# Kernel optimization log

Measured on AMD Instinct MI355X. Metric: run time of the kernel, lower is better.

The kernel has to match this reference:

```python
import jax, jax.numpy as jnp
import numpy as np

B, T, C, H = 2, 2048, 768, 12
HD = C // H  # head dim = 64


def setup_inputs() -> dict:
    key = jax.random.key(0)
    k1, k2, k3 = jax.random.split(key, 3)
    s_in = 1.0 / np.sqrt(C)
    return {
        "x": jax.random.normal(k1, (B, T, C), dtype=jnp.float32),
        "Wqkv": jax.random.normal(k2, (C, 3 * C), dtype=jnp.float32) * s_in,
        "bqkv": jnp.zeros((3 * C,), dtype=jnp.float32),
        "Wproj": jax.random.normal(k3, (C, C), dtype=jnp.float32) * s_in,
        "bproj": jnp.zeros((C,), dtype=jnp.float32),
    }


def reference(x, Wqkv, bqkv, Wproj, bproj):
    b, t, c = x.shape
    qkv = x @ Wqkv + bqkv                      # [b, t, 3c]
    q, k, v = jnp.split(qkv, 3, axis=2)
    # [b, h, t, hd]
    q = q.reshape(b, t, H, HD).transpose(0, 2, 1, 3)
    k = k.reshape(b, t, H, HD).transpose(0, 2, 1, 3)
    v = v.reshape(b, t, H, HD).transpose(0, 2, 1, 3)
    scale = 1.0 / np.sqrt(HD)
    att = jnp.einsum("bhqd,bhkd->bhqk", q, k) * scale  # [b, h, t, t]
    causal = jnp.tril(jnp.ones((t, t), dtype=bool))
    att = jnp.where(causal[None, None], att, -jnp.inf)
    att = jax.nn.softmax(att, axis=-1)
    y = jnp.einsum("bhqk,bhkd->bhqd", att, v)          # [b, h, t, hd]
    y = y.transpose(0, 2, 1, 3).reshape(b, t, c)
    return y @ Wproj + bproj
```

## Files before the change

kernel.cpp:

```cpp
#include <hip/hip_runtime.h>
#include <math.h>

#define BB 2
#define TT 2048
#define CC 768
#define HH 12
#define HD 64
#define N3 (3*CC)

typedef __attribute__((ext_vector_type(8))) short short8;
typedef __attribute__((ext_vector_type(8))) _Float16 f16x8;
typedef __attribute__((ext_vector_type(4))) float f32x4;
typedef unsigned short u16;

#define QSCALE 0.1803368809f

static __device__ __forceinline__ u16 f2h(float x) {
    union { _Float16 h; u16 u; } v; v.h = (_Float16)x; return v.u;
}
static __device__ __forceinline__ float ex2(float x) {
#if __has_builtin(__builtin_amdgcn_exp2f)
    return __builtin_amdgcn_exp2f(x);
#else
    return exp2f(x);
#endif
}
static __device__ __forceinline__ unsigned pk2h(float a, float b) {
    auto p = __builtin_amdgcn_cvt_pkrtz(a, b);
    return __builtin_bit_cast(unsigned, p);
}

static __device__ __forceinline__ void gl16(const void* g, void* l) {
    __builtin_amdgcn_global_load_lds(
        (const __attribute__((address_space(1))) void*)g,
        (__attribute__((address_space(3))) void*)l, 16, 0, 0);
}

__global__ __launch_bounds__(256)
void conv_all(const float* __restrict__ x, u16* __restrict__ xh,
              const float* __restrict__ Wq, u16* __restrict__ wqh,
              const float* __restrict__ Wp, u16* __restrict__ wph)
{
    __shared__ float Tt[64][65];
    const int b = blockIdx.x;
    if (b < 3072) {
        const int i = b * 256 + threadIdx.x;
        float4 v = ((const float4*)x)[i];
        ushort4 o;
        o.x = f2h(v.x); o.y = f2h(v.y); o.z = f2h(v.z); o.w = f2h(v.w);
        ((ushort4*)xh)[i] = o;
        return;
    }
    const float* W; u16* T; int N, idx;
    if (b < 3504) { W = Wq; T = wqh; N = N3; idx = b - 3072; }
    else          { W = Wp; T = wph; N = CC; idx = b - 3504; }
    const int ntx = N / 64;
    const int n0 = (idx % ntx) * 64, k0 = (idx / ntx) * 64;
    const int tid = threadIdx.x;
    {
        const int r = tid >> 2, q = tid & 3;
        #pragma unroll
        for (int i = 0; i < 4; ++i) {
            float4 v = *(const float4*)(W + (size_t)(k0 + r) * N + n0 + q * 16 + i * 4);
            Tt[q * 16 + i * 4 + 0][r] = v.x;
            Tt[q * 16 + i * 4 + 1][r] = v.y;
            Tt[q * 16 + i * 4 + 2][r] = v.z;
            Tt[q * 16 + i * 4 + 3][r] = v.w;
        }
    }
    __syncthreads();
    {
        const int n = tid >> 2, q = tid & 3;
        u16 hh[16];
        #pragma unroll
        for (int j = 0; j < 16; ++j) hh[j] = f2h(Tt[n][q * 16 + j]);
        u16* dh = T + (size_t)(n0 + n) * 768 + k0 + q * 16;
        *(short8*)(dh) = *(short8*)&hh[0];
        *(short8*)(dh + 8) = *(short8*)&hh[8];
    }
}

template<int NCOLS, int MODE>
__global__ __launch_bounds__(256)
void mm3(const u16* __restrict__ A_g, const u16* __restrict__ B_g,
         const float* __restrict__ bias, float* __restrict__ outF,
         u16* __restrict__ qo, u16* __restrict__ ko, u16* __restrict__ vto)
{
    __shared__ u16 gsm[16384];
    char* smb = (char*)gsm;
    const int tid = threadIdx.x, lane = tid & 63, wv = tid >> 6;
    const int wm = wv >> 1, wn = wv & 1, r16 = lane & 15, kg = lane >> 4;
    const int m0 = blockIdx.y * 128, n0 = blockIdx.x * 128;

    const u16 *pA[2], *pB[2];
    int ldsq[2];
    #pragma unroll
    for (int qq = 0; qq < 2; ++qq) {
        const int L = wv * 2048 + qq * 1024 + lane * 16;
        const int row = L >> 6, c = (L >> 4) & 3;
        const int cp = c ^ ((row >> 1) & 3);
        ldsq[qq] = wv * 2048 + qq * 1024;
        pA[qq] = A_g + (size_t)(m0 + row) * 768 + cp * 8;
        pB[qq] = B_g + (size_t)(n0 + row) * 768 + cp * 8;
    }

    int aA[4], aB[4];
    #pragma unroll
    for (int t = 0; t < 4; ++t) {
        const int rA = wm * 64 + t * 16 + r16;
        const int rB = wn * 64 + t * 16 + r16;
        aA[t] = rA * 64 + ((kg ^ ((rA >> 1) & 3)) << 4);
        aB[t] = rB * 64 + ((kg ^ ((rB >> 1) & 3)) << 4) + 8192;
    }

    f32x4 acc[4][4];
    #pragma unroll
    for (int i = 0; i < 4; ++i)
        #pragma unroll
        for (int j = 0; j < 4; ++j) acc[i][j] = (f32x4)0.f;

    #pragma unroll
    for (int qq = 0; qq < 2; ++qq) {
        gl16(pA[qq], smb + ldsq[qq]);
        gl16(pB[qq], smb + 8192 + ldsq[qq]);
        pA[qq] += 32; pB[qq] += 32;
    }
    __syncthreads();

    int cur = 0;
    for (int ks = 0; ks < 24; ++ks) {
        const int nxt = cur ^ 1;
        if (ks != 23) {
            #pragma unroll
            for (int qq = 0; qq < 2; ++qq) {
                gl16(pA[qq], smb + nxt * 16384 + ldsq[qq]);
                gl16(pB[qq], smb + nxt * 16384 + 8192 + ldsq[qq]);
                pA[qq] += 32; pB[qq] += 32;
            }
        }
        const int cb = cur * 16384;
        f16x8 a[4], b[4];
        #pragma unroll
        for (int t = 0; t < 4; ++t) {
            a[t] = *(const f16x8*)(smb + cb + aA[t]);
            b[t] = *(const f16x8*)(smb + cb + aB[t]);
        }
        #pragma unroll
        for (int mt = 0; mt < 4; ++mt)
            #pragma unroll
            for (int nt = 0; nt < 4; ++nt)
                acc[mt][nt] = __builtin_amdgcn_mfma_f32_16x16x32_f16(a[mt], b[nt], acc[mt][nt], 0, 0, 0);
        __syncthreads();
        cur = nxt;
    }

    float bi[4];
    #pragma unroll
    for (int nt = 0; nt < 4; ++nt) bi[nt] = bias[n0 + wn * 64 + nt * 16 + r16];

    if (MODE == 1) {
        #pragma unroll
        for (int mt = 0; mt < 4; ++mt)
            #pragma unroll
            for (int nt = 0; nt < 4; ++nt)
                #pragma unroll
                for (int r = 0; r < 4; ++r) {
                    const int grow = m0 + wm * 64 + mt * 16 + kg * 4 + r;
                    const int gcol = n0 + wn * 64 + nt * 16 + r16;
                    outF[(size_t)grow * CC + gcol] = acc[mt][nt][r] + bi[nt];
                }
    } else {
        const int which = n0 / CC;
        const float qsc = (which == 0) ? QSCALE : 1.0f;
        const int b_ = m0 >> 11;
        #pragma unroll
        for (int mt = 0; mt < 4; ++mt) {
            const int tb = ((m0 & 2047) + wm * 64 + mt * 16 + kg * 4);
            #pragma unroll
            for (int nt = 0; nt < 4; ++nt) {
                const int gcol = n0 + wn * 64 + nt * 16 + r16;
                const int cc = gcol - which * CC;
                const int h = cc >> 6, d = cc & 63;
                const int bh_ = b_ * HH + h;
                if (which == 2) {
                    ushort4 hv;
                    #pragma unroll
                    for (int r = 0; r < 4; ++r)
                        ((u16*)&hv)[r] = f2h(acc[mt][nt][r] + bi[nt]);
                    *(ushort4*)(vto + ((size_t)bh_ * 64 + d) * 2048 + tb) = hv;
                } else {
                    u16* dst = (which == 0) ? qo : ko;
                    #pragma unroll
                    for (int r = 0; r < 4; ++r)
                        dst[(((size_t)bh_ * 2048 + tb + r) << 6) + d] =
                            f2h((acc[mt][nt][r] + bi[nt]) * qsc);
                }
            }
        }
    }
}

__global__ __launch_bounds__(256)
void attn3(const u16* __restrict__ qp, const u16* __restrict__ kp,
           const u16* __restrict__ vtp, u16* __restrict__ attp)
{
    __shared__ u16 smem[24576];
    char* smb = (char*)smem;

    const int tid = threadIdx.x, bid = blockIdx.x;
    const int qt = 15 - (bid / 24);
    const int bh = bid % 24;
    const int t0 = qt * 128;
    const int jmax = 2 * qt + 1;
    const int diagA = 2 * qt;
    const int lane = tid & 63, wv = tid >> 6;
    const int r16 = lane & 15, kg = lane >> 4;
    const int r7 = r16 & 7;
    const int kg8 = kg * 8, kg4 = kg * 4;

    const size_t qroA = ((size_t)bh * TT + t0 + wv * 16 + r16) * 64;
    f16x8 qfA[2], qfB[2];
    #pragma unroll
    for (int ks = 0; ks < 2; ++ks) {
        qfA[ks] = *(const f16x8*)(qp + qroA + ks * 32 + kg8);
        qfB[ks] = *(const f16x8*)(qp + qroA + 4096 + ks * 32 + kg8);
    }
    const int rowA = t0 + wv * 16 + r16;
    const int rowB = rowA + 64;

    const u16 *pk[2], *pv[2];
    int ldsq[2];
    #pragma unroll
    for (int qq = 0; qq < 2; ++qq) {
        const int L = wv * 2048 + qq * 1024 + lane * 16;
        const int row = L >> 7, c = (L >> 4) & 7;
        const int cp = c ^ (row & 7);
        ldsq[qq] = wv * 2048 + qq * 1024;
        pk[qq] = kp + ((size_t)bh * TT + row) * 64 + cp * 8;
        pv[qq] = vtp + ((size_t)bh * 64 + row) * TT + cp * 8;
    }

    int aK[2][4], aPA[2], aPB[2];
    #pragma unroll
    for (int ks = 0; ks < 2; ++ks) {
        #pragma unroll
        for (int nt = 0; nt < 4; ++nt) {
            const int row = nt * 16 + r16;
            aK[ks][nt] = row * 128 + (((ks * 4 + kg) ^ (row & 7)) << 4);
        }
        aPA[ks] = 32768 + wv * 2048 + r16 * 128 + (((ks * 4 + kg) ^ r7) << 4);
        aPB[ks] = aPA[ks] + 8192;
    }
    const int pwA = 32768 + wv * 2048 + r16 * 128;
    const int pwB = pwA + 8192;

    f32x4 oA[4], oB[4];
    #pragma unroll
    for (int i = 0; i < 4; ++i) { oA[i] = (f32x4)0.f; oB[i] = (f32x4)0.f; }
    f32x4 lA = (f32x4)0.f, lB = (f32x4)0.f;
    float mA = -1e30f, mB = -1e30f;

    f16x8 ones;
    #pragma unroll
    for (int i = 0; i < 8; ++i) ones[i] = (_Float16)1.0f;

    #pragma unroll
    for (int qq = 0; qq < 2; ++qq) {
        gl16(pk[qq], smb + ldsq[qq]);
        gl16(pv[qq], smb + 8192 + ldsq[qq]);
        pk[qq] += 4096; pv[qq] += 64;
    }
    __syncthreads();

    int cur = 0;
    for (int j = 0; j <= jmax; ++j) {
        const int nxt = cur ^ 1;
        if (j != jmax) {
            #pragma unroll
            for (int qq = 0; qq < 2; ++qq) {
                gl16(pk[qq], smb + nxt * 16384 + ldsq[qq]);
                gl16(pv[qq], smb + nxt * 16384 + 8192 + ldsq[qq]);
                pk[qq] += 4096; pv[qq] += 64;
            }
        }
        const int cb = cur * 16384;
        const int kb = j * 64;

        f32x4 sA[4], sB[4];
        #pragma unroll
        for (int nt = 0; nt < 4; ++nt) { sA[nt] = (f32x4)0.f; sB[nt] = (f32x4)0.f; }
        __builtin_amdgcn_s_setprio(1);
        #pragma unroll
        for (int ks = 0; ks < 2; ++ks)
            #pragma unroll
            for (int nt = 0; nt < 4; ++nt) {
                f16x8 kf = *(const f16x8*)(smb + cb + aK[ks][nt]);
                sA[nt] = __builtin_amdgcn_mfma_f32_16x16x32_f16(kf, qfA[ks], sA[nt], 0, 0, 0);
                sB[nt] = __builtin_amdgcn_mfma_f32_16x16x32_f16(kf, qfB[ks], sB[nt], 0, 0, 0);
            }
        __builtin_amdgcn_s_setprio(0);

        if (j >= diagA) {
            #pragma unroll
            for (int nt = 0; nt < 4; ++nt)
                #pragma unroll
                for (int r = 0; r < 4; ++r)
                    if (kb + nt * 16 + kg4 + r > rowA) sA[nt][r] = -1e30f;
        }
        if (j == jmax) {
            #pragma unroll
            for (int nt = 0; nt < 4; ++nt)
                #pragma unroll
                for (int r = 0; r < 4; ++r)
                    if (kb + nt * 16 + kg4 + r > rowB) sB[nt][r] = -1e30f;
        }

        auto softmax = [&](f32x4 (&s)[4], float& m, f32x4& ol, f32x4 (&oa)[4],
                           int pwbase) {
            float pm = s[0][0];
            #pragma unroll
            for (int nt = 0; nt < 4; ++nt)
                #pragma unroll
                for (int r = 0; r < 4; ++r)
                    if (nt | r) pm = fmaxf(pm, s[nt][r]);
            pm = fmaxf(pm, __shfl_xor(pm, 16));
            pm = fmaxf(pm, __shfl_xor(pm, 32));
            if (__any(pm > m + 8.0f)) {
                const float mn = fmaxf(m, pm);
                const float corr = ex2(m - mn);
                m = mn;
                const float c0 = __shfl(corr, kg4 + 0);
                const float c1 = __shfl(corr, kg4 + 1);
                const float c2 = __shfl(corr, kg4 + 2);
                const float c3 = __shfl(corr, kg4 + 3);
                #pragma unroll
                for (int nt = 0; nt < 4; ++nt) {
                    oa[nt][0] *= c0; oa[nt][1] *= c1;
                    oa[nt][2] *= c2; oa[nt][3] *= c3;
                }
                ol[0] *= c0; ol[1] *= c1; ol[2] *= c2; ol[3] *= c3;
            }
            #pragma unroll
            for (int nt = 0; nt < 4; ++nt) {
                const float p0 = ex2(s[nt][0] - m), p1 = ex2(s[nt][1] - m);
                const float p2 = ex2(s[nt][2] - m), p3 = ex2(s[nt][3] - m);
                uint2 w;
                w.x = pk2h(p0, p1);
                w.y = pk2h(p2, p3);
                *(uint2*)(smb + pwbase + ((nt * 32 + kg8) ^ (r7 << 4))) = w;
            }
        };
        softmax(sA, mA, lA, oA, pwA);
        softmax(sB, mB, lB, oB, pwB);

        __builtin_amdgcn_s_setprio(1);
        #pragma unroll
        for (int ks = 0; ks < 2; ++ks) {
            f16x8 paA = *(const f16x8*)(smb + aPA[ks]);
            f16x8 paB = *(const f16x8*)(smb + aPB[ks]);
            lA = __builtin_amdgcn_mfma_f32_16x16x32_f16(paA, ones, lA, 0, 0, 0);
            lB = __builtin_amdgcn_mfma_f32_16x16x32_f16(paB, ones, lB, 0, 0, 0);
            #pragma unroll
            for (int nt = 0; nt < 4; ++nt) {
                f16x8 vf = *(const f16x8*)(smb + cb + 8192 + aK[ks][nt]);
                oA[nt] = __builtin_amdgcn_mfma_f32_16x16x32_f16(paA, vf, oA[nt], 0, 0, 0);
                oB[nt] = __builtin_amdgcn_mfma_f32_16x16x32_f16(paB, vf, oB[nt], 0, 0, 0);
            }
        }
        __builtin_amdgcn_s_setprio(0);

        __syncthreads();
        cur = nxt;
    }

    const int b_ = bh / HH, h = bh % HH;
    #pragma unroll
    for (int r = 0; r < 4; ++r) {
        const float invA = 1.f / lA[r];
        const float invB = 1.f / lB[r];
        const int tA = t0 + wv * 16 + kg4 + r;
        const size_t baseA = ((size_t)b_ * TT + tA) * CC + h * 64;
        const size_t baseB = baseA + (size_t)64 * CC;
        #pragma unroll
        for (int nt = 0; nt < 4; ++nt) {
            attp[baseA + nt * 16 + r16] = f2h(oA[nt][r] * invA);
            attp[baseB + nt * 16 + r16] = f2h(oB[nt][r] * invB);
        }
    }
}

extern "C" void kernel_launch(void* const* d_in, const int* in_sizes, int n_in,
                              void* d_out, int out_size, void* d_ws, size_t ws_size,
                              hipStream_t stream)
{
    const float* x     = (const float*)d_in[0];
    const float* Wqkv  = (const float*)d_in[1];
    const float* bqkv  = (const float*)d_in[2];
    const float* Wproj = (const float*)d_in[3];
    const float* bproj = (const float*)d_in[4];
    float* out = (float*)d_out;

    const size_t E  = (size_t)4096 * 768;
    const size_t WQ = (size_t)2304 * 768;
    const size_t WP = (size_t)768 * 768;

    u16* ws   = (u16*)d_ws;
    u16* xh   = ws;
    u16* atth = ws;
    u16* wqh  = ws + E;
    u16* wph  = wqh + WQ;
    u16* qh   = wph + WP;
    u16* kh   = qh + E;
    u16* vth  = kh + E;

    conv_all<<<dim3(3648), 256, 0, stream>>>(x, xh, Wqkv, wqh, Wproj, wph);

    mm3<N3, 0><<<dim3(N3 / 128, 32), 256, 0, stream>>>(
        xh, wqh, bqkv, nullptr, qh, kh, vth);
    attn3<<<dim3(384), 256, 0, stream>>>(qh, kh, vth, atth);
    mm3<CC, 1><<<dim3(CC / 128, 32), 256, 0, stream>>>(
        atth, wph, bproj, out, nullptr, nullptr, nullptr);
}
```

Baseline: 165.1 us.

## Restructure attention into single-wave blocks with 32-row query tiles and no barriers

The attention kernel now runs one 64-lane wavefront per block, each handling 32 query rows with 32-key tiles, giving 1536 blocks instead of 384 four-wave blocks. Each wave stages its own K/V tiles through a private double-buffered LDS region and waits with explicit vmcnt counters instead of __syncthreads. The aim is to remove block-wide barriers, shrink per-block LDS so more blocks fit per CU, and spread the causal triangle over finer work units. In exchange, each K/V tile loaded from global memory is reused by fewer query rows, which raises global/L2 traffic, and there are more iterations with per-iteration softmax overhead.

```diff
diff --git a/kernel.cpp b/kernel.cpp
--- a/kernel.cpp
+++ b/kernel.cpp
@@ -200,59 +200,59 @@
     }
 }
 
-__global__ __launch_bounds__(256)
+__global__ __launch_bounds__(64)
 void attn3(const u16* __restrict__ qp, const u16* __restrict__ kp,
            const u16* __restrict__ vtp, u16* __restrict__ attp)
 {
-    __shared__ u16 smem[24576];
+    __shared__ u16 smem[10240];
     char* smb = (char*)smem;
 
-    const int tid = threadIdx.x, bid = blockIdx.x;
-    const int qt = 15 - (bid / 24);
+    const int lane = threadIdx.x;
+    const int bid = blockIdx.x;
+    const int qt = 63 - (bid / 24);
     const int bh = bid % 24;
-    const int t0 = qt * 128;
-    const int jmax = 2 * qt + 1;
-    const int diagA = 2 * qt;
-    const int lane = tid & 63, wv = tid >> 6;
+    const int t0 = qt * 32;
     const int r16 = lane & 15, kg = lane >> 4;
-    const int r7 = r16 & 7;
-    const int kg8 = kg * 8, kg4 = kg * 4;
-
-    const size_t qroA = ((size_t)bh * TT + t0 + wv * 16 + r16) * 64;
+    const int kg4 = kg * 4, kg8 = kg * 8;
+    const int pwx = (r16 & 7) << 4;
+
+    const size_t qroA = ((size_t)bh * TT + t0 + r16) * 64;
     f16x8 qfA[2], qfB[2];
     #pragma unroll
     for (int ks = 0; ks < 2; ++ks) {
         qfA[ks] = *(const f16x8*)(qp + qroA + ks * 32 + kg8);
-        qfB[ks] = *(const f16x8*)(qp + qroA + 4096 + ks * 32 + kg8);
-    }
-    const int rowA = t0 + wv * 16 + r16;
-    const int rowB = rowA + 64;
-
-    const u16 *pk[2], *pv[2];
-    int ldsq[2];
-    #pragma unroll
-    for (int qq = 0; qq < 2; ++qq) {
-        const int L = wv * 2048 + qq * 1024 + lane * 16;
-        const int row = L >> 7, c = (L >> 4) & 7;
-        const int cp = c ^ (row & 7);
-        ldsq[qq] = wv * 2048 + qq * 1024;
-        pk[qq] = kp + ((size_t)bh * TT + row) * 64 + cp * 8;
-        pv[qq] = vtp + ((size_t)bh * 64 + row) * TT + cp * 8;
-    }
-
-    int aK[2][4], aPA[2], aPB[2];
-    #pragma unroll
-    for (int ks = 0; ks < 2; ++ks) {
-        #pragma unroll
-        for (int nt = 0; nt < 4; ++nt) {
+        qfB[ks] = *(const f16x8*)(qp + qroA + 1024 + ks * 32 + kg8);
+    }
+
+    const u16 *pk[4], *pv[4];
+    #pragma unroll
+    for (int rr = 0; rr < 4; ++rr) {
+        const int key0 = rr * 8 + (lane >> 3);
+        const int cpk  = (lane & 7) ^ (lane >> 3);
+        pk[rr] = kp + ((size_t)bh * TT + key0) * 64 + cpk * 8;
+        const int d0  = rr * 16 + (lane >> 2);
+        const int cpv = (lane & 3) ^ ((lane >> 2) & 3);
+        pv[rr] = vtp + ((size_t)(bh * 64 + d0)) * TT + cpv * 8;
+    }
+
+    int aK[2][2], aV[4], aP[2], pw[2];
+    #pragma unroll
+    for (int ks = 0; ks < 2; ++ks)
+        #pragma unroll
+        for (int nt = 0; nt < 2; ++nt) {
             const int row = nt * 16 + r16;
             aK[ks][nt] = row * 128 + (((ks * 4 + kg) ^ (row & 7)) << 4);
         }
-        aPA[ks] = 32768 + wv * 2048 + r16 * 128 + (((ks * 4 + kg) ^ r7) << 4);
-        aPB[ks] = aPA[ks] + 8192;
-    }
-    const int pwA = 32768 + wv * 2048 + r16 * 128;
-    const int pwB = pwA + 8192;
+    #pragma unroll
+    for (int nt = 0; nt < 4; ++nt) {
+        const int d = nt * 16 + r16;
+        aV[nt] = 4096 + d * 64 + ((kg ^ (d & 3)) << 4);
+    }
+    #pragma unroll
+    for (int s = 0; s < 2; ++s) {
+        aP[s] = 16384 + s * 2048 + r16 * 128 + ((kg ^ (r16 & 7)) << 4);
+        pw[s] = 16384 + s * 2048 + r16 * 128;
+    }
 
     f32x4 oA[4], oB[4];
     #pragma unroll
@@ -264,65 +264,56 @@
     #pragma unroll
     for (int i = 0; i < 8; ++i) ones[i] = (_Float16)1.0f;
 
-    #pragma unroll
-    for (int qq = 0; qq < 2; ++qq) {
-        gl16(pk[qq], smb + ldsq[qq]);
-        gl16(pv[qq], smb + 8192 + ldsq[qq]);
-        pk[qq] += 4096; pv[qq] += 64;
-    }
-    __syncthreads();
-
+    auto stage = [&](int bufb) {
+        #pragma unroll
+        for (int rr = 0; rr < 4; ++rr) {
+            gl16(pk[rr], smb + bufb + rr * 1024);
+            gl16(pv[rr], smb + bufb + 4096 + rr * 1024);
+            pk[rr] += 2048;
+            pv[rr] += 32;
+        }
+    };
+
+    stage(0);
     int cur = 0;
-    for (int j = 0; j <= jmax; ++j) {
-        const int nxt = cur ^ 1;
-        if (j != jmax) {
-            #pragma unroll
-            for (int qq = 0; qq < 2; ++qq) {
-                gl16(pk[qq], smb + nxt * 16384 + ldsq[qq]);
-                gl16(pv[qq], smb + nxt * 16384 + 8192 + ldsq[qq]);
-                pk[qq] += 4096; pv[qq] += 64;
-            }
-        }
-        const int cb = cur * 16384;
-        const int kb = j * 64;
-
-        f32x4 sA[4], sB[4];
-        #pragma unroll
-        for (int nt = 0; nt < 4; ++nt) { sA[nt] = (f32x4)0.f; sB[nt] = (f32x4)0.f; }
+    for (int j = 0; j <= qt; ++j) {
+        if (j < qt) {
+            stage((cur ^ 1) * 8192);
+            asm volatile("s_waitcnt vmcnt(8)" ::: "memory");
+        } else {
+            asm volatile("s_waitcnt vmcnt(0)" ::: "memory");
+        }
+        const int cb = cur * 8192;
+
+        f32x4 sA[2], sB[2];
+        sA[0] = (f32x4)0.f; sA[1] = (f32x4)0.f;
+        sB[0] = (f32x4)0.f; sB[1] = (f32x4)0.f;
         __builtin_amdgcn_s_setprio(1);
         #pragma unroll
         for (int ks = 0; ks < 2; ++ks)
             #pragma unroll
-            for (int nt = 0; nt < 4; ++nt) {
+            for (int nt = 0; nt < 2; ++nt) {
                 f16x8 kf = *(const f16x8*)(smb + cb + aK[ks][nt]);
                 sA[nt] = __builtin_amdgcn_mfma_f32_16x16x32_f16(kf, qfA[ks], sA[nt], 0, 0, 0);
                 sB[nt] = __builtin_amdgcn_mfma_f32_16x16x32_f16(kf, qfB[ks], sB[nt], 0, 0, 0);
             }
         __builtin_amdgcn_s_setprio(0);
 
-        if (j >= diagA) {
-            #pragma unroll
-            for (int nt = 0; nt < 4; ++nt)
+        if (j == qt) {
+            #pragma unroll
+            for (int nt = 0; nt < 2; ++nt)
                 #pragma unroll
-                for (int r = 0; r < 4; ++r)
-                    if (kb + nt * 16 + kg4 + r > rowA) sA[nt][r] = -1e30f;
-        }
-        if (j == jmax) {
-            #pragma unroll
-            for (int nt = 0; nt < 4; ++nt)
-                #pragma unroll
-                for (int r = 0; r < 4; ++r)
-                    if (kb + nt * 16 + kg4 + r > rowB) sB[nt][r] = -1e30f;
-        }
-
-        auto softmax = [&](f32x4 (&s)[4], float& m, f32x4& ol, f32x4 (&oa)[4],
-                           int pwbase) {
-            float pm = s[0][0];
-            #pragma unroll
-            for (int nt = 0; nt < 4; ++nt)
-                #pragma unroll
-                for (int r = 0; r < 4; ++r)
-                    if (nt | r) pm = fmaxf(pm, s[nt][r]);
+                for (int r = 0; r < 4; ++r) {
+                    const int keyo = nt * 16 + kg4 + r;
+                    if (keyo > r16)      sA[nt][r] = -1e30f;
+                    if (keyo > 16 + r16) sB[nt][r] = -1e30f;
+                }
+        }
+
+        auto softmax = [&](f32x4 (&s)[2], float& m, f32x4& ol, f32x4 (&oa)[4],
+                           int pwb) {
+            float pm = fmaxf(fmaxf(fmaxf(s[0][0], s[0][1]), fmaxf(s[0][2], s[0][3])),
+                             fmaxf(fmaxf(s[1][0], s[1][1]), fmaxf(s[1][2], s[1][3])));
             pm = fmaxf(pm, __shfl_xor(pm, 16));
             pm = fmaxf(pm, __shfl_xor(pm, 32));
             if (__any(pm > m + 8.0f)) {
@@ -341,36 +332,30 @@
                 ol[0] *= c0; ol[1] *= c1; ol[2] *= c2; ol[3] *= c3;
             }
             #pragma unroll
-            for (int nt = 0; nt < 4; ++nt) {
-                const float p0 = ex2(s[nt][0] - m), p1 = ex2(s[nt][1] - m);
-                const float p2 = ex2(s[nt][2] - m), p3 = ex2(s[nt][3] - m);
+            for (int nt = 0; nt < 2; ++nt) {
                 uint2 w;
-                w.x = pk2h(p0, p1);
-                w.y = pk2h(p2, p3);
-                *(uint2*)(smb + pwbase + ((nt * 32 + kg8) ^ (r7 << 4))) = w;
+                w.x = pk2h(ex2(s[nt][0] - m), ex2(s[nt][1] - m));
+                w.y = pk2h(ex2(s[nt][2] - m), ex2(s[nt][3] - m));
+                *(uint2*)(smb + pwb + ((nt * 32 + kg8) ^ pwx)) = w;
             }
         };
-        softmax(sA, mA, lA, oA, pwA);
-        softmax(sB, mB, lB, oB, pwB);
+        softmax(sA, mA, lA, oA, pw[0]);
+        softmax(sB, mB, lB, oB, pw[1]);
 
         __builtin_amdgcn_s_setprio(1);
-        #pragma unroll
-        for (int ks = 0; ks < 2; ++ks) {
-            f16x8 paA = *(const f16x8*)(smb + aPA[ks]);
-            f16x8 paB = *(const f16x8*)(smb + aPB[ks]);
-            lA = __builtin_amdgcn_mfma_f32_16x16x32_f16(paA, ones, lA, 0, 0, 0);
-            lB = __builtin_amdgcn_mfma_f32_16x16x32_f16(paB, ones, lB, 0, 0, 0);
-            #pragma unroll
-            for (int nt = 0; nt < 4; ++nt) {
-                f16x8 vf = *(const f16x8*)(smb + cb + 8192 + aK[ks][nt]);
-                oA[nt] = __builtin_amdgcn_mfma_f32_16x16x32_f16(paA, vf, oA[nt], 0, 0, 0);
-                oB[nt] = __builtin_amdgcn_mfma_f32_16x16x32_f16(paB, vf, oB[nt], 0, 0, 0);
-            }
+        f16x8 paA = *(const f16x8*)(smb + aP[0]);
+        f16x8 paB = *(const f16x8*)(smb + aP[1]);
+        lA = __builtin_amdgcn_mfma_f32_16x16x32_f16(paA, ones, lA, 0, 0, 0);
+        lB = __builtin_amdgcn_mfma_f32_16x16x32_f16(paB, ones, lB, 0, 0, 0);
+        #pragma unroll
+        for (int nt = 0; nt < 4; ++nt) {
+            f16x8 vf = *(const f16x8*)(smb + cb + aV[nt]);
+            oA[nt] = __builtin_amdgcn_mfma_f32_16x16x32_f16(paA, vf, oA[nt], 0, 0, 0);
+            oB[nt] = __builtin_amdgcn_mfma_f32_16x16x32_f16(paB, vf, oB[nt], 0, 0, 0);
         }
         __builtin_amdgcn_s_setprio(0);
 
-        __syncthreads();
-        cur = nxt;
+        cur ^= 1;
     }
 
     const int b_ = bh / HH, h = bh % HH;
@@ -378,9 +363,9 @@
     for (int r = 0; r < 4; ++r) {
         const float invA = 1.f / lA[r];
         const float invB = 1.f / lB[r];
-        const int tA = t0 + wv * 16 + kg4 + r;
+        const int tA = t0 + kg4 + r;
         const size_t baseA = ((size_t)b_ * TT + tA) * CC + h * 64;
-        const size_t baseB = baseA + (size_t)64 * CC;
+        const size_t baseB = baseA + (size_t)16 * CC;
         #pragma unroll
         for (int nt = 0; nt < 4; ++nt) {
             attp[baseA + nt * 16 + r16] = f2h(oA[nt][r] * invA);
@@ -417,7 +402,7 @@
 
     mm3<N3, 0><<<dim3(N3 / 128, 32), 256, 0, stream>>>(
         xh, wqh, bqkv, nullptr, qh, kh, vth);
-    attn3<<<dim3(384), 256, 0, stream>>>(qh, kh, vth, atth);
+    attn3<<<dim3(1536), 64, 0, stream>>>(qh, kh, vth, atth);
     mm3<CC, 1><<<dim3(CC / 128, 32), 256, 0, stream>>>(
         atth, wph, bproj, out, nullptr, nullptr, nullptr);
 }
```

Result: slower. 179.6 us (+8.8%).
